# Optimization experiments

Measured on AMD Instinct MI355X. Metric: run time of the kernel, lower is better.

Reference implementation:

```python
import jax, jax.numpy as jnp
import numpy as np

N, E, H, C = 100000, 1600000, 4, 32  # nodes, edges, heads, per-head channels
F_IN, F_HID, F_OUT = 128, 32, 16
NEG_SLOPE = 0.2


def setup_inputs() -> dict:
    key = jax.random.key(0)
    ks = jax.random.split(key, 16)
    s = 0.05
    return {
        "x": jax.random.normal(ks[0], (N, F_IN), jnp.float32),
        "edge_index": jax.random.randint(ks[1], (2, E), 0, N, jnp.int32),
        "W0": jax.random.normal(ks[2], (F_IN, H * C), jnp.float32) * s,
        "att_src0": jax.random.normal(ks[3], (H, C), jnp.float32) * s,
        "att_dst0": jax.random.normal(ks[4], (H, C), jnp.float32) * s,
        "b0": jax.random.normal(ks[5], (H * C,), jnp.float32) * s,
        "W1": jax.random.normal(ks[6], (H * C, H * C), jnp.float32) * s,
        "att_src1": jax.random.normal(ks[7], (H, C), jnp.float32) * s,
        "att_dst1": jax.random.normal(ks[8], (H, C), jnp.float32) * s,
        "b1": jax.random.normal(ks[9], (H * C,), jnp.float32) * s,
        "Wm1": jax.random.normal(ks[10], (H * C, F_HID), jnp.float32) * s,
        "bm1": jax.random.normal(ks[11], (F_HID,), jnp.float32) * s,
        "Wm2": jax.random.normal(ks[12], (F_HID, F_OUT), jnp.float32) * s,
        "bm2": jax.random.normal(ks[13], (F_OUT,), jnp.float32) * s,
    }


def gat_layer(x, src, dst, W, att_src, att_dst, bias):
    n = x.shape[0]
    h = (x @ W).reshape(n, H, C)                       # [N,H,C]
    a_src = jnp.einsum("nhc,hc->nh", h, att_src)       # [N,H]
    a_dst = jnp.einsum("nhc,hc->nh", h, att_dst)       # [N,H]
    e = a_src[src] + a_dst[dst]                        # [E,H]
    e = jnp.where(e > 0, e, NEG_SLOPE * e)             # leaky_relu(0.2)
    m = jax.ops.segment_max(e, dst, num_segments=n)    # [N,H] segment softmax
    ee = jnp.exp(e - m[dst])
    z = jax.ops.segment_sum(ee, dst, num_segments=n)
    alpha = ee / z[dst]                                # [E,H]
    msg = alpha[:, :, None] * h[src]                   # [E,H,C]
    out = jax.ops.segment_sum(msg, dst, num_segments=n)  # [N,H,C]
    return out.reshape(n, H * C) + bias


def reference(x, edge_index, W0, att_src0, att_dst0, b0,
              W1, att_src1, att_dst1, b1, Wm1, bm1, Wm2, bm2):
    src, dst = edge_index[0], edge_index[1]
    x = jax.nn.relu(gat_layer(x, src, dst, W0, att_src0, att_dst0, b0))
    x = jax.nn.relu(gat_layer(x, src, dst, W1, att_src1, att_dst1, b1))
    x = jax.nn.relu(x @ Wm1 + bm1)
    return x @ Wm2 + bm2
```

## Files before the change

### kernel.cpp

```cpp
#include <hip/hip_runtime.h>
#include <hip/hip_bf16.h>

#define NEG 0.2f
#define BCAP 8192

typedef __attribute__((ext_vector_type(8))) short short8v;
typedef __attribute__((ext_vector_type(4))) float f32x4;

static __device__ __forceinline__ float bf2f(unsigned int u16){
  return __uint_as_float(u16 << 16);
}
static __device__ __forceinline__ unsigned short f2bf(float f){
  __hip_bfloat16 h = __float2bfloat16(f);
  return *reinterpret_cast<unsigned short*>(&h);
}

#define CHUNK 2048
#define PER_T 8


static __device__ __forceinline__ void binpass_body(
    const int* __restrict__ src, const int* __restrict__ dst,
    int* __restrict__ bfill, unsigned int* __restrict__ pairs, int E, int NB,
    int blk, int* lcnt, int* lbase)
{
  int t = threadIdx.x;
  int ebase = blk * CHUNK;
  for (int j=t; j<NB; j+=256) lcnt[j]=0;
  __syncthreads();
  unsigned int pv[PER_T]; int pb[PER_T];
  #pragma unroll
  for (int k=0;k<PER_T;++k){
    int i = ebase + t + k*256;
    pb[k] = -1;
    if (i < E){
      int d = dst[i];
      int s = src[i];
      pb[k] = d >> 8;
      pv[k] = ((unsigned int)s << 8) | (unsigned int)(d & 255);
      atomicAdd(&lcnt[pb[k]], 1);
    }
  }
  __syncthreads();
  for (int j=t; j<NB; j+=256){
    int c = lcnt[j];
    lbase[j] = c ? atomicAdd(&bfill[j], c) : 0;
    lcnt[j] = 0;
  }
  __syncthreads();
  #pragma unroll
  for (int k=0;k<PER_T;++k){
    if (pb[k] >= 0){
      int ofs = atomicAdd(&lcnt[pb[k]], 1);
      int idx = lbase[pb[k]] + ofs;
      if (idx < BCAP)
        pairs[(size_t)pb[k]*BCAP + idx] = pv[k];
    }
  }
}

template<int IN_BF16>
static __device__ __forceinline__ void gemm_att_body(
    const void* __restrict__ xin_, const unsigned short* __restrict__ wt,
    const float* __restrict__ atts, const float* __restrict__ attd,
    unsigned short* __restrict__ hb, float* __restrict__ as_, float* __restrict__ ad_,
    int n, int blk, unsigned short* xls)
{
  int t = threadIdx.x;
  int base = blk*64;
  int nrem = n - base;
  if (IN_BF16){
    const uint4* Xb = reinterpret_cast<const uint4*>(xin_);
    #pragma unroll
    for (int j=0;j<4;++j){
      int i = t + j*256;
      int row = i >> 4, c16 = i & 15;
      uint4 v = (row < nrem) ? Xb[(size_t)(base+row)*16 + c16]
                             : make_uint4(0,0,0,0);
      int addr = row*256 + ((c16*16) ^ ((row&7)<<4));
      *reinterpret_cast<uint4*>(reinterpret_cast<char*>(xls) + addr) = v;
    }
  } else {
    const float4* X4 = reinterpret_cast<const float4*>(xin_);
    #pragma unroll
    for (int j=0;j<8;++j){
      int i = t + j*256;
      int row = i >> 5, cb = i & 31;
      float4 v = (row < nrem) ? X4[(size_t)(base+row)*32 + cb] : make_float4(0.f,0.f,0.f,0.f);
      unsigned int p0 = (unsigned int)f2bf(v.x) | ((unsigned int)f2bf(v.y)<<16);
      unsigned int p1 = (unsigned int)f2bf(v.z) | ((unsigned int)f2bf(v.w)<<16);
      int addr = row*256 + ((cb*8) ^ ((row&7)<<4));
      *reinterpret_cast<uint2*>(reinterpret_cast<char*>(xls) + addr) = make_uint2(p0,p1);
    }
  }
  __syncthreads();
  int w = t >> 6;
  int l = t & 63;
  int l15 = l & 15, l4 = l >> 4;
  int n0 = w*32;
  short8v bfr[2][4];
  #pragma unroll
  for (int nt=0;nt<2;++nt){
    const unsigned short* bp = wt + (size_t)(n0 + nt*16 + l15)*128 + l4*8;
    #pragma unroll
    for (int kk=0;kk<4;++kk)
      bfr[nt][kk] = *reinterpret_cast<const short8v*>(bp + kk*32);
  }
  f32x4 acc[4][2];
  #pragma unroll
  for (int mt=0;mt<4;++mt)
    #pragma unroll
    for (int nt=0;nt<2;++nt)
      acc[mt][nt] = (f32x4){0.f,0.f,0.f,0.f};
  #pragma unroll
  for (int kk=0;kk<4;++kk){
    short8v afr[4];
    #pragma unroll
    for (int mt=0;mt<4;++mt){
      int row = mt*16 + l15;
      int addr = row*256 + ((kk*64 + l4*16) ^ ((row&7)<<4));
      afr[mt] = *reinterpret_cast<const short8v*>(reinterpret_cast<char*>(xls) + addr);
    }
    #pragma unroll
    for (int mt=0;mt<4;++mt)
      #pragma unroll
      for (int nt=0;nt<2;++nt)
        acc[mt][nt] = __builtin_amdgcn_mfma_f32_16x16x32_bf16(afr[mt], bfr[nt][kk], acc[mt][nt], 0, 0, 0);
  }
  float av0 = atts[n0 + l15],    av1 = atts[n0 + 16 + l15];
  float dv0 = attd[n0 + l15],    dv1 = attd[n0 + 16 + l15];
  #pragma unroll
  for (int mt=0;mt<4;++mt){
    #pragma unroll
    for (int r=0;r<4;++r){
      float ps = acc[mt][0][r]*av0 + acc[mt][1][r]*av1;
      float pd = acc[mt][0][r]*dv0 + acc[mt][1][r]*dv1;
      ps += __shfl_xor(ps,1); ps += __shfl_xor(ps,2);
      ps += __shfl_xor(ps,4); ps += __shfl_xor(ps,8);
      pd += __shfl_xor(pd,1); pd += __shfl_xor(pd,2);
      pd += __shfl_xor(pd,4); pd += __shfl_xor(pd,8);
      int node = base + mt*16 + l4*4 + r;
      if (l15==0 && node < n){
        as_[node*4 + w] = ps;
        ad_[node*4 + w] = pd;
      }
    }
  }
  __syncthreads();
  #pragma unroll
  for (int mt=0;mt<4;++mt)
    #pragma unroll
    for (int nt=0;nt<2;++nt)
      #pragma unroll
      for (int r=0;r<4;++r){
        int row = mt*16 + l4*4 + r;
        int col = n0 + nt*16 + l15;
        xls[row*128 + col] = f2bf(acc[mt][nt][r]);
      }
  __syncthreads();
  const uint4* xsrc = reinterpret_cast<const uint4*>(xls);
  uint4* hdst = reinterpret_cast<uint4*>(hb + (size_t)base*128);
  #pragma unroll
  for (int j=0;j<4;++j){
    int i = t + j*256;
    int row = i >> 4;
    if (row < nrem) hdst[i] = xsrc[i];
  }
}


__global__ __launch_bounds__(256) void k_wconv(
    const float* __restrict__ W0, const float* __restrict__ W1,
    unsigned short* __restrict__ wt0, unsigned short* __restrict__ wt1)
{
  int b = blockIdx.x;
  const float* W = (b < 64) ? W0 : W1;
  unsigned short* wt = (b < 64) ? wt0 : wt1;
  int i = (b & 63)*256 + threadIdx.x;
  int k = i >> 7, nn = i & 127;
  wt[nn*128 + k] = f2bf(W[i]);
}

__global__ __launch_bounds__(256) void k_gemm1_binpass(
    const float* __restrict__ xin, const unsigned short* __restrict__ wt,
    const float* __restrict__ atts, const float* __restrict__ attd,
    unsigned short* __restrict__ hb, float* __restrict__ as_, float* __restrict__ ad_,
    int n, int nG,
    const int* __restrict__ src, const int* __restrict__ dst,
    int* __restrict__ bfill, unsigned int* __restrict__ pairs, int E, int NB)
{
  __shared__ __align__(16) unsigned short xls[64*128];
  __shared__ int lcnt[512];
  __shared__ int lbase[512];
  int b = blockIdx.x;
  if (b < nG){
    gemm_att_body<0>(xin, wt, atts, attd, hb, as_, ad_, n, b, xls);
  } else {
    binpass_body(src, dst, bfill, pairs, E, NB, b - nG, lcnt, lbase);
  }
}

__global__ __launch_bounds__(256) void k_gemm2(
    const unsigned short* __restrict__ xin, const unsigned short* __restrict__ wt,
    const float* __restrict__ atts, const float* __restrict__ attd,
    unsigned short* __restrict__ hb, float* __restrict__ as_, float* __restrict__ ad_, int n)
{
  __shared__ __align__(16) unsigned short xls[64*128];
  gemm_att_body<1>(xin, wt, atts, attd, hb, as_, ad_, n, blockIdx.x, xls);
}

__global__ __launch_bounds__(256) void k_csr(
    const unsigned int* __restrict__ pairs, const int* __restrict__ bfill,
    int2* __restrict__ rp2, int* __restrict__ csr, int n)
{
  __shared__ int lc[256];
  __shared__ int sd[256];
  __shared__ int rp[257];
  int b = blockIdx.x;
  int base = b << 8;
  int t = threadIdx.x;
  int cnt = n - base; if (cnt > 256) cnt = 256;
  int cbase = b * BCAP;
  int ecnt = bfill[b]; if (ecnt > BCAP) ecnt = BCAP;
  lc[t]=0; __syncthreads();
  for (int i = t; i < ecnt; i += 256)
    atomicAdd(&lc[pairs[cbase + i] & 255u], 1);
  __syncthreads();
  int v = lc[t];
  sd[t]=v; __syncthreads();
  for (int off=1; off<256; off<<=1){
    int x = (t>=off) ? sd[t-off] : 0;
    __syncthreads();
    sd[t] += x;
    __syncthreads();
  }
  rp[t+1] = cbase + sd[t];
  if (t==0) rp[0] = cbase;
  lc[t] = 0;
  __syncthreads();
  if (t < cnt) rp2[base + t] = make_int2(rp[t], rp[t+1]);
  for (int i = t; i < ecnt; i += 256){
    unsigned int p = pairs[cbase + i];
    int d = (int)(p & 255u);
    int ofs = atomicAdd(&lc[d], 1);
    csr[rp[d] + ofs] = (int)(p >> 8);
  }
}

__global__ __launch_bounds__(256) void k_aggr(
    const unsigned short* __restrict__ hb, const float* __restrict__ as_,
    const float* __restrict__ ad_, const int2* __restrict__ rp2,
    const int* __restrict__ csr, const float* __restrict__ bias,
    unsigned short* __restrict__ out, int n)
{
  int node = (int)((blockIdx.x*(size_t)blockDim.x + threadIdx.x) >> 5);
  int li = threadIdx.x & 31;
  if (node >= n) return;
  int c0 = li*4;
  int head = li >> 3;
  const uint2* __restrict__ h2 = reinterpret_cast<const uint2*>(hb);
  float adn = ad_[node*4 + head];
  int2 be = rp2[node];
  int beg = be.x, end = be.y;
  int deg = end - beg;
  float4 acc = make_float4(0.f,0.f,0.f,0.f);
  float z = 0.f;
  int nfull = deg & ~3;
  int lim = beg + nfull;
  int i = beg;
  int s0=0,s1=0,s2=0,s3=0;
  if (i < lim){ s0=csr[i]; s1=csr[i+1]; s2=csr[i+2]; s3=csr[i+3]; }
  for (; i < lim; ){
    int ni = i + 4;
    int t0=0,t1=0,t2=0,t3=0;
    if (ni < lim){ t0=csr[ni]; t1=csr[ni+1]; t2=csr[ni+2]; t3=csr[ni+3]; }
    float e0 = as_[s0*4+head];
    float e1 = as_[s1*4+head];
    float e2 = as_[s2*4+head];
    float e3 = as_[s3*4+head];
    uint2 p0 = h2[s0*32 + li];
    uint2 p1 = h2[s1*32 + li];
    uint2 p2 = h2[s2*32 + li];
    uint2 p3 = h2[s3*32 + li];
    e0 += adn; e1 += adn; e2 += adn; e3 += adn;
    e0 = (e0>0.f)?e0:NEG*e0;
    e1 = (e1>0.f)?e1:NEG*e1;
    e2 = (e2>0.f)?e2:NEG*e2;
    e3 = (e3>0.f)?e3:NEG*e3;
    float x0 = __expf(e0);
    float x1 = __expf(e1);
    float x2 = __expf(e2);
    float x3 = __expf(e3);
    z += (x0+x1)+(x2+x3);
    acc.x = fmaf(x0, bf2f(p0.x & 0xffffu), acc.x);
    acc.y = fmaf(x0, bf2f(p0.x >> 16),     acc.y);
    acc.z = fmaf(x0, bf2f(p0.y & 0xffffu), acc.z);
    acc.w = fmaf(x0, bf2f(p0.y >> 16),     acc.w);
    acc.x = fmaf(x1, bf2f(p1.x & 0xffffu), acc.x);
    acc.y = fmaf(x1, bf2f(p1.x >> 16),     acc.y);
    acc.z = fmaf(x1, bf2f(p1.y & 0xffffu), acc.z);
    acc.w = fmaf(x1, bf2f(p1.y >> 16),     acc.w);
    acc.x = fmaf(x2, bf2f(p2.x & 0xffffu), acc.x);
    acc.y = fmaf(x2, bf2f(p2.x >> 16),     acc.y);
    acc.z = fmaf(x2, bf2f(p2.y & 0xffffu), acc.z);
    acc.w = fmaf(x2, bf2f(p2.y >> 16),     acc.w);
    acc.x = fmaf(x3, bf2f(p3.x & 0xffffu), acc.x);
    acc.y = fmaf(x3, bf2f(p3.x >> 16),     acc.y);
    acc.z = fmaf(x3, bf2f(p3.y & 0xffffu), acc.z);
    acc.w = fmaf(x3, bf2f(p3.y >> 16),     acc.w);
    i = ni; s0=t0; s1=t1; s2=t2; s3=t3;
  }
  for (int j = beg + nfull; j < end; ++j){
    int s = csr[j];
    float e = as_[s*4+head] + adn;
    e = (e>0.f)?e:NEG*e;
    float ee = __expf(e);
    z += ee;
    uint2 pv = h2[s*32 + li];
    acc.x = fmaf(ee, bf2f(pv.x & 0xffffu), acc.x);
    acc.y = fmaf(ee, bf2f(pv.x >> 16),     acc.y);
    acc.z = fmaf(ee, bf2f(pv.y & 0xffffu), acc.z);
    acc.w = fmaf(ee, bf2f(pv.y >> 16),     acc.w);
  }
  float4 o;
  if (deg > 0){
    float rz = 1.f/z;
    o.x = fmaxf(fmaf(acc.x,rz,bias[c0  ]), 0.f);
    o.y = fmaxf(fmaf(acc.y,rz,bias[c0+1]), 0.f);
    o.z = fmaxf(fmaf(acc.z,rz,bias[c0+2]), 0.f);
    o.w = fmaxf(fmaf(acc.w,rz,bias[c0+3]), 0.f);
  } else {
    o.x = fmaxf(bias[c0  ], 0.f);
    o.y = fmaxf(bias[c0+1], 0.f);
    o.z = fmaxf(bias[c0+2], 0.f);
    o.w = fmaxf(bias[c0+3], 0.f);
  }
  unsigned int lo = (unsigned int)f2bf(o.x) | ((unsigned int)f2bf(o.y)<<16);
  unsigned int hi = (unsigned int)f2bf(o.z) | ((unsigned int)f2bf(o.w)<<16);
  reinterpret_cast<uint2*>(out)[node*32 + li] = make_uint2(lo,hi);
}

__global__ __launch_bounds__(256) void k_mlp(
    const unsigned short* __restrict__ xb, const float* __restrict__ Wm1, const float* __restrict__ bm1,
    const float* __restrict__ Wm2, const float* __restrict__ bm2,
    float* __restrict__ out, int n)
{
  __shared__ float xs[64*129];
  __shared__ float w1s[128*32];
  __shared__ float hs[64*33];
  __shared__ float w2s[32*16];
  __shared__ float b1s[32];
  __shared__ float b2s[16];
  int t = threadIdx.x;
  int base = blockIdx.x*64;
  const uint4* Xb = reinterpret_cast<const uint4*>(xb);
  #pragma unroll
  for (int j=0;j<4;++j){
    int i = t + j*256;
    int row = i >> 4, seg = i & 15;
    uint4 v = (base+row < n) ? Xb[(size_t)(base+row)*16 + seg] : make_uint4(0,0,0,0);
    float* xp = &xs[row*129 + seg*8];
    xp[0] = bf2f(v.x & 0xffffu); xp[1] = bf2f(v.x >> 16);
    xp[2] = bf2f(v.y & 0xffffu); xp[3] = bf2f(v.y >> 16);
    xp[4] = bf2f(v.z & 0xffffu); xp[5] = bf2f(v.z >> 16);
    xp[6] = bf2f(v.w & 0xffffu); xp[7] = bf2f(v.w >> 16);
  }
  for (int i=t; i<128*32; i+=256) w1s[i]=Wm1[i];
  for (int i=t; i<32*16;  i+=256) w2s[i]=Wm2[i];
  if (t<32) b1s[t]=bm1[t];
  if (t<16) b2s[t]=bm2[t];
  __syncthreads();
  int l = t&63, g = t>>6;
  float hid[8];
  #pragma unroll
  for (int j=0;j<8;++j) hid[j]=0.f;
  for (int k=0;k<128;++k){
    float xk = xs[l*129+k];
    #pragma unroll
    for (int j=0;j<8;++j) hid[j] = fmaf(xk, w1s[k*32 + g*8 + j], hid[j]);
  }
  #pragma unroll
  for (int j=0;j<8;++j) hs[l*33 + g*8 + j] = fmaxf(hid[j] + b1s[g*8+j], 0.f);
  __syncthreads();
  float o[4] = {0.f,0.f,0.f,0.f};
  for (int k=0;k<32;++k){
    float xv = hs[l*33+k];
    #pragma unroll
    for (int j=0;j<4;++j) o[j] = fmaf(xv, w2s[k*16 + g*4 + j], o[j]);
  }
  int node = base + l;
  if (node < n){
    #pragma unroll
    for (int j=0;j<4;++j) out[(size_t)node*16 + g*4 + j] = o[j] + b2s[g*4+j];
  }
}

extern "C" void kernel_launch(void* const* d_in, const int* in_sizes, int n_in,
                              void* d_out, int out_size, void* d_ws, size_t ws_size,
                              hipStream_t stream)
{
  const float* x   = (const float*)d_in[0];
  const int*   ei  = (const int*)  d_in[1];
  const float* W0  = (const float*)d_in[2];
  const float* as0 = (const float*)d_in[3];
  const float* ad0 = (const float*)d_in[4];
  const float* b0  = (const float*)d_in[5];
  const float* W1  = (const float*)d_in[6];
  const float* as1 = (const float*)d_in[7];
  const float* ad1 = (const float*)d_in[8];
  const float* b1  = (const float*)d_in[9];
  const float* Wm1 = (const float*)d_in[10];
  const float* bm1 = (const float*)d_in[11];
  const float* Wm2 = (const float*)d_in[12];
  const float* bm2 = (const float*)d_in[13];
  int N = in_sizes[0]/128;
  int E = in_sizes[1]/2;
  const int* srcI = ei;
  const int* dstI = ei + E;

  char* ws = (char*)d_ws;
  size_t off = 0;
  auto alloc = [&](size_t bytes)->void*{
    void* p = ws + off; off += (bytes + 255) & ~(size_t)255; return p;
  };
  int NB = (N + 255) >> 8;
  unsigned short* hbuf = (unsigned short*)alloc((size_t)N*128*2);
  unsigned short* xbuf = (unsigned short*)alloc((size_t)N*128*2);
  float* asb   = (float*)alloc((size_t)N*4*4);
  float* adb   = (float*)alloc((size_t)N*4*4);
  int2* rp2    = (int2*)alloc((size_t)N*8);
  int* bfill   = (int*)alloc((size_t)NB*4);
  int* csr     = (int*)alloc((size_t)NB*BCAP*4);
  unsigned int* pairs = (unsigned int*)alloc((size_t)NB*BCAP*4);
  unsigned short* wt0 = (unsigned short*)alloc(128*128*2);
  unsigned short* wt1 = (unsigned short*)alloc(128*128*2);
  (void)ws_size; (void)n_in; (void)out_size;

  int gC = (E + CHUNK - 1) / CHUNK;
  int gG = (N+63)/64;
  int gA = (int)(((size_t)N*32 + 255)/256);

  hipMemsetAsync(bfill, 0, (size_t)NB*4, stream);
  k_wconv       <<<128,256,0,stream>>>(W0, W1, wt0, wt1);
  k_gemm1_binpass<<<gG+gC,256,0,stream>>>(x, wt0, as0, ad0, hbuf, asb, adb, N, gG,
                                          srcI, dstI, bfill, pairs, E, NB);
  k_csr         <<<NB,256,0,stream>>>(pairs, bfill, rp2, csr, N);
  k_aggr        <<<gA,256,0,stream>>>(hbuf, asb, adb, rp2, csr, b0, xbuf, N);
  k_gemm2       <<<gG,256,0,stream>>>(xbuf, wt1, as1, ad1, hbuf, asb, adb, N);
  k_aggr        <<<gA,256,0,stream>>>(hbuf, asb, adb, rp2, csr, b1, xbuf, N);
  k_mlp         <<<gG,256,0,stream>>>(xbuf, Wm1, bm1, Wm2, bm2, (float*)d_out, N);
}
```

Measured before the change: 266.1 us.

## Widen aggregation lanes to 16B loads, fold memset into wconv, alias shared buffers

The aggregation kernel now uses 16 lanes per node, each loading a uint4 (8 bf16 channels) instead of a uint2, so each edge's feature gather uses wider loads and half as many lanes. The per-edge index and attention work is spread over fewer lanes, and each lane holds more accumulators. The bfill memset becomes an extra block of the weight-conversion kernel, dropping one enqueued operation. The binning pass and the MLP reuse existing shared buffers to cut shared-memory use, which may raise occupancy; the MLP pays for this with an extra __syncthreads.

```diff
diff --git a/kernel.cpp b/kernel.cpp
--- a/kernel.cpp
+++ b/kernel.cpp
@@ -171,12 +171,18 @@
 
 __global__ __launch_bounds__(256) void k_wconv(
     const float* __restrict__ W0, const float* __restrict__ W1,
-    unsigned short* __restrict__ wt0, unsigned short* __restrict__ wt1)
+    unsigned short* __restrict__ wt0, unsigned short* __restrict__ wt1,
+    int* __restrict__ bfill, int NB)
 {
   int b = blockIdx.x;
+  int t = threadIdx.x;
+  if (b == 128){
+    for (int j=t; j<NB; j+=256) bfill[j] = 0;
+    return;
+  }
   const float* W = (b < 64) ? W0 : W1;
   unsigned short* wt = (b < 64) ? wt0 : wt1;
-  int i = (b & 63)*256 + threadIdx.x;
+  int i = (b & 63)*256 + t;
   int k = i >> 7, nn = i & 127;
   wt[nn*128 + k] = f2bf(W[i]);
 }
@@ -190,12 +196,12 @@
     int* __restrict__ bfill, unsigned int* __restrict__ pairs, int E, int NB)
 {
   __shared__ __align__(16) unsigned short xls[64*128];
-  __shared__ int lcnt[512];
-  __shared__ int lbase[512];
   int b = blockIdx.x;
   if (b < nG){
     gemm_att_body<0>(xin, wt, atts, attd, hb, as_, ad_, n, b, xls);
   } else {
+    int* lcnt  = reinterpret_cast<int*>(xls);
+    int* lbase = reinterpret_cast<int*>(xls) + 512;
     binpass_body(src, dst, bfill, pairs, E, NB, b - nG, lcnt, lbase);
   }
 }
@@ -253,17 +259,19 @@
     const int* __restrict__ csr, const float* __restrict__ bias,
     unsigned short* __restrict__ out, int n)
 {
-  int node = (int)((blockIdx.x*(size_t)blockDim.x + threadIdx.x) >> 5);
-  int li = threadIdx.x & 31;
+  int node = (int)((blockIdx.x*(size_t)blockDim.x + threadIdx.x) >> 4);
+  int li = threadIdx.x & 15;
   if (node >= n) return;
-  int c0 = li*4;
-  int head = li >> 3;
-  const uint2* __restrict__ h2 = reinterpret_cast<const uint2*>(hb);
+  int c0 = li*8;
+  int head = li >> 2;
+  const uint4* __restrict__ h4 = reinterpret_cast<const uint4*>(hb);
   float adn = ad_[node*4 + head];
   int2 be = rp2[node];
   int beg = be.x, end = be.y;
   int deg = end - beg;
-  float4 acc = make_float4(0.f,0.f,0.f,0.f);
+  float acc[8];
+  #pragma unroll
+  for (int q=0;q<8;++q) acc[q]=0.f;
   float z = 0.f;
   int nfull = deg & ~3;
   int lim = beg + nfull;
@@ -278,10 +286,10 @@
     float e1 = as_[s1*4+head];
     float e2 = as_[s2*4+head];
     float e3 = as_[s3*4+head];
-    uint2 p0 = h2[s0*32 + li];
-    uint2 p1 = h2[s1*32 + li];
-    uint2 p2 = h2[s2*32 + li];
-    uint2 p3 = h2[s3*32 + li];
+    uint4 p0 = h4[s0*16 + li];
+    uint4 p1 = h4[s1*16 + li];
+    uint4 p2 = h4[s2*16 + li];
+    uint4 p3 = h4[s3*16 + li];
     e0 += adn; e1 += adn; e2 += adn; e3 += adn;
     e0 = (e0>0.f)?e0:NEG*e0;
     e1 = (e1>0.f)?e1:NEG*e1;
@@ -292,22 +300,30 @@
     float x2 = __expf(e2);
     float x3 = __expf(e3);
     z += (x0+x1)+(x2+x3);
-    acc.x = fmaf(x0, bf2f(p0.x & 0xffffu), acc.x);
-    acc.y = fmaf(x0, bf2f(p0.x >> 16),     acc.y);
-    acc.z = fmaf(x0, bf2f(p0.y & 0xffffu), acc.z);
-    acc.w = fmaf(x0, bf2f(p0.y >> 16),     acc.w);
-    acc.x = fmaf(x1, bf2f(p1.x & 0xffffu), acc.x);
-    acc.y = fmaf(x1, bf2f(p1.x >> 16),     acc.y);
-    acc.z = fmaf(x1, bf2f(p1.y & 0xffffu), acc.z);
-    acc.w = fmaf(x1, bf2f(p1.y >> 16),     acc.w);
-    acc.x = fmaf(x2, bf2f(p2.x & 0xffffu), acc.x);
-    acc.y = fmaf(x2, bf2f(p2.x >> 16),     acc.y);
-    acc.z = fmaf(x2, bf2f(p2.y & 0xffffu), acc.z);
-    acc.w = fmaf(x2, bf2f(p2.y >> 16),     acc.w);
-    acc.x = fmaf(x3, bf2f(p3.x & 0xffffu), acc.x);
-    acc.y = fmaf(x3, bf2f(p3.x >> 16),     acc.y);
-    acc.z = fmaf(x3, bf2f(p3.y & 0xffffu), acc.z);
-    acc.w = fmaf(x3, bf2f(p3.y >> 16),     acc.w);
+    unsigned int w0[4] = {p0.x,p0.y,p0.z,p0.w};
+    unsigned int w1[4] = {p1.x,p1.y,p1.z,p1.w};
+    unsigned int w2[4] = {p2.x,p2.y,p2.z,p2.w};
+    unsigned int w3[4] = {p3.x,p3.y,p3.z,p3.w};
+    #pragma unroll
+    for (int q=0;q<4;++q){
+      acc[2*q]   = fmaf(x0, bf2f(w0[q] & 0xffffu), acc[2*q]);
+      acc[2*q+1] = fmaf(x0, bf2f(w0[q] >> 16),     acc[2*q+1]);
+    }
+    #pragma unroll
+    for (int q=0;q<4;++q){
+      acc[2*q]   = fmaf(x1, bf2f(w1[q] & 0xffffu), acc[2*q]);
+      acc[2*q+1] = fmaf(x1, bf2f(w1[q] >> 16),     acc[2*q+1]);
+    }
+    #pragma unroll
+    for (int q=0;q<4;++q){
+      acc[2*q]   = fmaf(x2, bf2f(w2[q] & 0xffffu), acc[2*q]);
+      acc[2*q+1] = fmaf(x2, bf2f(w2[q] >> 16),     acc[2*q+1]);
+    }
+    #pragma unroll
+    for (int q=0;q<4;++q){
+      acc[2*q]   = fmaf(x3, bf2f(w3[q] & 0xffffu), acc[2*q]);
+      acc[2*q+1] = fmaf(x3, bf2f(w3[q] >> 16),     acc[2*q+1]);
+    }
     i = ni; s0=t0; s1=t1; s2=t2; s3=t3;
   }
   for (int j = beg + nfull; j < end; ++j){
@@ -316,28 +332,29 @@
     e = (e>0.f)?e:NEG*e;
     float ee = __expf(e);
     z += ee;
-    uint2 pv = h2[s*32 + li];
-    acc.x = fmaf(ee, bf2f(pv.x & 0xffffu), acc.x);
-    acc.y = fmaf(ee, bf2f(pv.x >> 16),     acc.y);
-    acc.z = fmaf(ee, bf2f(pv.y & 0xffffu), acc.z);
-    acc.w = fmaf(ee, bf2f(pv.y >> 16),     acc.w);
-  }
-  float4 o;
+    uint4 pv = h4[s*16 + li];
+    unsigned int wv[4] = {pv.x,pv.y,pv.z,pv.w};
+    #pragma unroll
+    for (int q=0;q<4;++q){
+      acc[2*q]   = fmaf(ee, bf2f(wv[q] & 0xffffu), acc[2*q]);
+      acc[2*q+1] = fmaf(ee, bf2f(wv[q] >> 16),     acc[2*q+1]);
+    }
+  }
+  float o[8];
   if (deg > 0){
     float rz = 1.f/z;
-    o.x = fmaxf(fmaf(acc.x,rz,bias[c0  ]), 0.f);
-    o.y = fmaxf(fmaf(acc.y,rz,bias[c0+1]), 0.f);
-    o.z = fmaxf(fmaf(acc.z,rz,bias[c0+2]), 0.f);
-    o.w = fmaxf(fmaf(acc.w,rz,bias[c0+3]), 0.f);
+    #pragma unroll
+    for (int q=0;q<8;++q) o[q] = fmaxf(fmaf(acc[q], rz, bias[c0+q]), 0.f);
   } else {
-    o.x = fmaxf(bias[c0  ], 0.f);
-    o.y = fmaxf(bias[c0+1], 0.f);
-    o.z = fmaxf(bias[c0+2], 0.f);
-    o.w = fmaxf(bias[c0+3], 0.f);
-  }
-  unsigned int lo = (unsigned int)f2bf(o.x) | ((unsigned int)f2bf(o.y)<<16);
-  unsigned int hi = (unsigned int)f2bf(o.z) | ((unsigned int)f2bf(o.w)<<16);
-  reinterpret_cast<uint2*>(out)[node*32 + li] = make_uint2(lo,hi);
+    #pragma unroll
+    for (int q=0;q<8;++q) o[q] = fmaxf(bias[c0+q], 0.f);
+  }
+  uint4 ov;
+  ov.x = (unsigned int)f2bf(o[0]) | ((unsigned int)f2bf(o[1])<<16);
+  ov.y = (unsigned int)f2bf(o[2]) | ((unsigned int)f2bf(o[3])<<16);
+  ov.z = (unsigned int)f2bf(o[4]) | ((unsigned int)f2bf(o[5])<<16);
+  ov.w = (unsigned int)f2bf(o[6]) | ((unsigned int)f2bf(o[7])<<16);
+  reinterpret_cast<uint4*>(out)[(size_t)node*16 + li] = ov;
 }
 
 __global__ __launch_bounds__(256) void k_mlp(
@@ -347,7 +364,6 @@
 {
   __shared__ float xs[64*129];
   __shared__ float w1s[128*32];
-  __shared__ float hs[64*33];
   __shared__ float w2s[32*16];
   __shared__ float b1s[32];
   __shared__ float b2s[16];
@@ -379,6 +395,8 @@
     #pragma unroll
     for (int j=0;j<8;++j) hid[j] = fmaf(xk, w1s[k*32 + g*8 + j], hid[j]);
   }
+  __syncthreads();
+  float* hs = xs;
   #pragma unroll
   for (int j=0;j<8;++j) hs[l*33 + g*8 + j] = fmaxf(hid[j] + b1s[g*8+j], 0.f);
   __syncthreads();
@@ -438,10 +456,9 @@
 
   int gC = (E + CHUNK - 1) / CHUNK;
   int gG = (N+63)/64;
-  int gA = (int)(((size_t)N*32 + 255)/256);
-
-  hipMemsetAsync(bfill, 0, (size_t)NB*4, stream);
-  k_wconv       <<<128,256,0,stream>>>(W0, W1, wt0, wt1);
+  int gA = (int)(((size_t)N*16 + 255)/256);
+
+  k_wconv       <<<129,256,0,stream>>>(W0, W1, wt0, wt1, bfill, NB);
   k_gemm1_binpass<<<gG+gC,256,0,stream>>>(x, wt0, as0, ad0, hbuf, asb, adb, N, gG,
                                           srcI, dstI, bfill, pairs, E, NB);
   k_csr         <<<NB,256,0,stream>>>(pairs, bfill, rp2, csr, N);
```

Result: faster. 256.2 us (median of 2 runs) (-3.7%).
